# Kernel optimization log

Hardware: AMD Instinct MI355X
Metric: run time of the kernel (lower is better)

The kernel has to match this reference:

```python
import jax, jax.numpy as jnp
import numpy as np

B, T, C, HS = 4, 4096, 1024, 64


def setup_inputs() -> dict:
    key = jax.random.key(0)
    kx, kq, kk, kv = jax.random.split(key, 4)
    x = jax.random.normal(kx, (B, T, C), dtype=jnp.float32)
    s = 1.0 / np.sqrt(C)
    Wq = jax.random.normal(kq, (C, HS), dtype=jnp.float32) * s
    Wk = jax.random.normal(kk, (C, HS), dtype=jnp.float32) * s
    Wv = jax.random.normal(kv, (C, HS), dtype=jnp.float32) * s
    return {"x": x, "Wq": Wq, "Wk": Wk, "Wv": Wv}


def reference(x, Wq, Wk, Wv):
    # q,k,v: [B, T, HS]
    q = x @ Wq
    k = x @ Wk
    v = x @ Wv
    scale = k.shape[-1] ** -0.5
    # full T x T causal attention scores, as the torch module materializes
    scores = jnp.einsum('bqh,bkh->bqk', q, k) * scale  # [B, T, T]
    t = x.shape[1]
    causal = jnp.tril(jnp.ones((t, t), dtype=bool))
    scores = jnp.where(causal[None, :, :], scores, -jnp.inf)
    wei = jax.nn.softmax(scores, axis=-1)  # dropout = 0.0 (eval)
    out = jnp.einsum('bqk,bkh->bqh', wei, v)  # [B, T, HS]
    return out
```

## Files before the change

kernel.cpp:

```cpp
#include <hip/hip_runtime.h>
#include <math.h>

#define BB 4
#define TT 4096
#define CC 1024
#define HS 64
#define MM (BB*TT)
#define KSPLIT 8

typedef __attribute__((ext_vector_type(8))) short short8;
typedef __attribute__((ext_vector_type(4))) float f32x4;
typedef __attribute__((ext_vector_type(4))) unsigned short ushort4v;

__device__ __forceinline__ unsigned short f2bf(float f) {
    union { float f; unsigned u; } v; v.f = f;
    return (unsigned short)((v.u + 0x7fffu + ((v.u >> 16) & 1u)) >> 16);
}

__device__ __forceinline__ unsigned cvt_pk_bf16(float lo, float hi) {
    unsigned r;
    asm("v_cvt_pk_bf16_f32 %0, %1, %2" : "=v"(r) : "v"(lo), "v"(hi));
    return r;
}

__global__ __launch_bounds__(256) void prep_kernel(
    const float* __restrict__ Wq, const float* __restrict__ Wk,
    const float* __restrict__ Wv, unsigned short* __restrict__ Wt)
{
    const int which = blockIdx.x >> 4;
    const int k0 = (blockIdx.x & 15) * 64;
    const float* __restrict__ W = (which == 0) ? Wq : (which == 1) ? Wk : Wv;
    const float scale = (which == 0) ? 0.125f : 1.0f;
    __shared__ unsigned short lds[64][65];
    const int t = threadIdx.x;
    #pragma unroll
    for (int i = 0; i < 16; i++) {
        int idx = t + 256 * i;
        int r = idx >> 6, n = idx & 63;
        lds[r][n] = f2bf(W[(size_t)(k0 + r) * 64 + n] * scale);
    }
    __syncthreads();
    #pragma unroll
    for (int i = 0; i < 16; i++) {
        int idx = t + 256 * i;
        int n = idx >> 6, r = idx & 63;
        Wt[(which << 16) + (n << 10) + k0 + r] = lds[r][n];
    }
}

__global__ __launch_bounds__(256, 2) void qkv_mfma(
    const float* __restrict__ x, const unsigned short* __restrict__ Wt,
    unsigned short* __restrict__ qb, unsigned short* __restrict__ kb,
    unsigned short* __restrict__ vT)
{
    const int rt = blockIdx.x;
    __shared__ unsigned short xs[32][136];
    __shared__ unsigned short ws[192][136];

    const int t = threadIdx.x;
    const int w = t >> 6;
    const int lane = t & 63;
    const int quad = lane >> 4;
    const int c = lane & 15;

    float4 xreg[4];
    short8 wreg[12];
    #pragma unroll
    for (int i = 0; i < 4; i++) {
        int idx = t + 256 * i;
        int r = idx >> 5, c4 = (idx & 31) * 4;
        xreg[i] = *(const float4*)(x + (size_t)(rt * 32 + r) * CC + c4);
    }
    #pragma unroll
    for (int i = 0; i < 12; i++) {
        int idx = t + 256 * i;
        int n = idx >> 4, c8 = (idx & 15) * 8;
        wreg[i] = *(const short8*)(Wt + (size_t)n * CC + c8);
    }

    f32x4 acc[2][3];
    #pragma unroll
    for (int mt = 0; mt < 2; mt++)
        #pragma unroll
        for (int j = 0; j < 3; j++) acc[mt][j] = (f32x4){0.f, 0.f, 0.f, 0.f};

    for (int k0 = 0; k0 < CC; k0 += 128) {
        __syncthreads();
        #pragma unroll
        for (int i = 0; i < 4; i++) {
            int idx = t + 256 * i;
            int r = idx >> 5, c4 = (idx & 31) * 4;
            ushort4v p = { f2bf(xreg[i].x), f2bf(xreg[i].y), f2bf(xreg[i].z), f2bf(xreg[i].w) };
            *(ushort4v*)&xs[r][c4] = p;
        }
        #pragma unroll
        for (int i = 0; i < 12; i++) {
            int idx = t + 256 * i;
            int n = idx >> 4, c8 = (idx & 15) * 8;
            *(short8*)&ws[n][c8] = wreg[i];
        }
        if (k0 + 128 < CC) {
            #pragma unroll
            for (int i = 0; i < 4; i++) {
                int idx = t + 256 * i;
                int r = idx >> 5, c4 = (idx & 31) * 4;
                xreg[i] = *(const float4*)(x + (size_t)(rt * 32 + r) * CC + k0 + 128 + c4);
            }
            #pragma unroll
            for (int i = 0; i < 12; i++) {
                int idx = t + 256 * i;
                int n = idx >> 4, c8 = (idx & 15) * 8;
                wreg[i] = *(const short8*)(Wt + (size_t)n * CC + k0 + 128 + c8);
            }
        }
        __syncthreads();
        #pragma unroll
        for (int ks = 0; ks < 4; ks++) {
            short8 af[2], bf[3];
            #pragma unroll
            for (int mt = 0; mt < 2; mt++)
                af[mt] = *(const short8*)&xs[16 * mt + c][ks * 32 + quad * 8];
            #pragma unroll
            for (int j = 0; j < 3; j++)
                bf[j] = *(const short8*)&ws[16 * (w + 4 * j) + c][ks * 32 + quad * 8];
            #pragma unroll
            for (int mt = 0; mt < 2; mt++)
                #pragma unroll
                for (int j = 0; j < 3; j++)
                    acc[mt][j] = __builtin_amdgcn_mfma_f32_16x16x32_bf16(af[mt], bf[j], acc[mt][j], 0, 0, 0);
        }
    }

    __syncthreads();
    unsigned short (*vtb)[72] = (unsigned short (*)[72])ws;
    #pragma unroll
    for (int mt = 0; mt < 2; mt++) {
        int grow = rt * 32 + 16 * mt + quad * 4;
        #pragma unroll
        for (int reg = 0; reg < 4; reg++) {
            qb[(size_t)(grow + reg) * HS + 16 * w + c] = f2bf(acc[mt][0][reg]);
            kb[(size_t)(grow + reg) * HS + 16 * w + c] = f2bf(acc[mt][1][reg]);
            vtb[16 * w + c][16 * mt + quad * 4 + reg] = f2bf(acc[mt][2][reg]);
        }
    }
    __syncthreads();
    {
        const int b  = rt >> 7;
        const int t0 = (rt & 127) * 32;
        int d = t >> 2, c8 = (t & 3) * 8;
        short8 v0 = *(const short8*)&vtb[d][c8];
        *(short8*)(vT + (size_t)b * HS * TT + (size_t)d * TT + t0 + c8) = v0;
    }
}

__global__ __launch_bounds__(256, 4) void attn_mfma(
    const unsigned short* __restrict__ qb, const unsigned short* __restrict__ kb,
    const unsigned short* __restrict__ vT, float* __restrict__ Opart,
    float* __restrict__ lpart)
{
    const int bid = blockIdx.x;
    const int qt = (TT / 128 - 1) - (bid >> 5);
    const int j  = (bid >> 2) & 7;
    const int b  = bid & 3;

    __shared__ unsigned short ks[64][72];
    __shared__ unsigned short vt[64][72];
    __shared__ unsigned short ps[4][32][72];

    const int t = threadIdx.x;
    const int w = t >> 6;
    const int lane = t & 63;
    const int quad = lane >> 4;
    const int c = lane & 15;
    const int qrow = qt * 128 + 32 * w;

    short8 aq[2][2];
    #pragma unroll
    for (int mt = 0; mt < 2; mt++)
        #pragma unroll
        for (int kstep = 0; kstep < 2; kstep++)
            aq[mt][kstep] = *(const short8*)(qb + (size_t)(b * TT + qrow + 16 * mt + c) * HS + kstep * 32 + quad * 8);

    const int lastkt = 2 * qt + 1;
    const int nkt = (lastkt >= j) ? ((lastkt - j) >> 3) + 1 : 0;
    const unsigned short* Kb = kb + (size_t)b * TT * HS;
    const unsigned short* Vb = vT + (size_t)b * HS * TT;

    const int srow = t >> 3;
    const int sc8  = (t & 7) * 8;

    short8 kreg[2], vreg[2];
    if (nkt > 0) {
        const int kt0 = j * 64;
        #pragma unroll
        for (int i = 0; i < 2; i++) {
            kreg[i] = *(const short8*)(Kb + (size_t)(kt0 + srow + 32 * i) * HS + sc8);
            vreg[i] = *(const short8*)(Vb + (size_t)(srow + 32 * i) * TT + kt0 + sc8);
        }
    }

    float l[2][4] = {{0.f,0.f,0.f,0.f},{0.f,0.f,0.f,0.f}};
    f32x4 oacc[2][4];
    #pragma unroll
    for (int mt = 0; mt < 2; mt++)
        #pragma unroll
        for (int dt = 0; dt < 4; dt++) oacc[mt][dt] = (f32x4){0.f, 0.f, 0.f, 0.f};

#define SCORE_ST(MASKC) do { \
    _Pragma("unroll") \
    for (int st = 0; st < 4; st++) { \
        f32x4 s[2]; \
        s[0] = (f32x4){0.f,0.f,0.f,0.f}; s[1] = (f32x4){0.f,0.f,0.f,0.f}; \
        _Pragma("unroll") \
        for (int kstep = 0; kstep < 2; kstep++) { \
            short8 bf = *(const short8*)&ks[16 * st + c][kstep * 32 + quad * 8]; \
            s[0] = __builtin_amdgcn_mfma_f32_16x16x32_bf16(aq[0][kstep], bf, s[0], 0, 0, 0); \
            s[1] = __builtin_amdgcn_mfma_f32_16x16x32_bf16(aq[1][kstep], bf, s[1], 0, 0, 0); \
        } \
        _Pragma("unroll") \
        for (int mt = 0; mt < 2; mt++) { \
            _Pragma("unroll") \
            for (int reg = 0; reg < 4; reg++) { \
                int kg = kt0 + 16 * st + c; (void)kg; \
                int qg = qrow + 16 * mt + quad * 4 + reg; (void)qg; \
                float p = (MASKC) ? __expf(s[mt][reg]) : 0.f; \
                s[mt][reg] = p; \
                l[mt][reg] += p; \
            } \
            unsigned p01 = cvt_pk_bf16(s[mt][0], s[mt][1]); \
            unsigned p23 = cvt_pk_bf16(s[mt][2], s[mt][3]); \
            ps[w][16 * mt + quad * 4 + 0][16 * st + c] = (unsigned short)p01; \
            ps[w][16 * mt + quad * 4 + 1][16 * st + c] = (unsigned short)(p01 >> 16); \
            ps[w][16 * mt + quad * 4 + 2][16 * st + c] = (unsigned short)p23; \
            ps[w][16 * mt + quad * 4 + 3][16 * st + c] = (unsigned short)(p23 >> 16); \
        } \
    } } while (0)

    for (int i = 0; i < nkt; i++) {
        const int kt = j + KSPLIT * i;
        const int kt0 = kt * 64;
        __syncthreads();
        #pragma unroll
        for (int ii = 0; ii < 2; ii++) {
            *(short8*)&ks[srow + 32 * ii][sc8] = kreg[ii];
            *(short8*)&vt[srow + 32 * ii][sc8] = vreg[ii];
        }
        __syncthreads();

        if (i + 1 < nkt) {
            const int nb = kt0 + KSPLIT * 64;
            #pragma unroll
            for (int ii = 0; ii < 2; ii++) {
                kreg[ii] = *(const short8*)(Kb + (size_t)(nb + srow + 32 * ii) * HS + sc8);
                vreg[ii] = *(const short8*)(Vb + (size_t)(srow + 32 * ii) * TT + nb + sc8);
            }
        }

        if (kt0 > qrow + 31) continue;

        if (kt >= 2 * qt) {
            SCORE_ST(kg <= qg);
        } else {
            SCORE_ST(1);
        }

        #pragma unroll
        for (int kstep = 0; kstep < 2; kstep++) {
            short8 ap[2];
            #pragma unroll
            for (int mt = 0; mt < 2; mt++)
                ap[mt] = *(const short8*)&ps[w][16 * mt + c][kstep * 32 + quad * 8];
            #pragma unroll
            for (int dt = 0; dt < 4; dt++) {
                short8 bv = *(const short8*)&vt[16 * dt + c][kstep * 32 + quad * 8];
                oacc[0][dt] = __builtin_amdgcn_mfma_f32_16x16x32_bf16(ap[0], bv, oacc[0][dt], 0, 0, 0);
                oacc[1][dt] = __builtin_amdgcn_mfma_f32_16x16x32_bf16(ap[1], bv, oacc[1][dt], 0, 0, 0);
            }
        }
    }
#undef SCORE_ST

    #pragma unroll
    for (int mt = 0; mt < 2; mt++)
        #pragma unroll
        for (int reg = 0; reg < 4; reg++)
            #pragma unroll
            for (int msk = 1; msk < 16; msk <<= 1)
                l[mt][reg] += __shfl_xor(l[mt][reg], msk);

    float* __restrict__ Oj = Opart + (size_t)j * MM * HS;
    #pragma unroll
    for (int mt = 0; mt < 2; mt++)
        #pragma unroll
        for (int dt = 0; dt < 4; dt++)
            #pragma unroll
            for (int reg = 0; reg < 4; reg++)
                Oj[(size_t)(b * TT + qrow + 16 * mt + quad * 4 + reg) * HS + 16 * dt + c] = oacc[mt][dt][reg];
    if (c == 0)
        #pragma unroll
        for (int mt = 0; mt < 2; mt++)
            #pragma unroll
            for (int reg = 0; reg < 4; reg++)
                lpart[(size_t)j * MM + b * TT + qrow + 16 * mt + quad * 4 + reg] = l[mt][reg];
}

__global__ __launch_bounds__(256) void combine_kernel(
    const float* __restrict__ Opart, const float* __restrict__ lpart,
    float* __restrict__ out)
{
    const int id = blockIdx.x * 256 + threadIdx.x;
    const int row = id >> 4;
    float l = 0.f;
    #pragma unroll
    for (int j = 0; j < KSPLIT; j++) l += lpart[(size_t)j * MM + row];
    const float4* O = (const float4*)Opart;
    const size_t stride = (size_t)MM * HS / 4;
    float4 r = {0.f, 0.f, 0.f, 0.f};
    #pragma unroll
    for (int j = 0; j < KSPLIT; j++) {
        float4 a = O[id + (size_t)j * stride];
        r.x += a.x; r.y += a.y; r.z += a.z; r.w += a.w;
    }
    float inv = 1.f / l;
    r.x *= inv; r.y *= inv; r.z *= inv; r.w *= inv;
    ((float4*)out)[id] = r;
}

extern "C" void kernel_launch(void* const* d_in, const int* in_sizes, int n_in,
                              void* d_out, int out_size, void* d_ws, size_t ws_size,
                              hipStream_t stream) {
    const float* x  = (const float*)d_in[0];
    const float* Wq = (const float*)d_in[1];
    const float* Wk = (const float*)d_in[2];
    const float* Wv = (const float*)d_in[3];
    float* out = (float*)d_out;

    unsigned short* Wt   = (unsigned short*)d_ws;
    unsigned short* qbuf = Wt + 3 * 64 * 1024;
    unsigned short* kbuf = qbuf + (size_t)MM * HS;
    unsigned short* vTb  = kbuf + (size_t)MM * HS;
    float* Opart = (float*)(vTb + (size_t)MM * HS);
    float* lpart = Opart + (size_t)KSPLIT * MM * HS;

    prep_kernel<<<48, 256, 0, stream>>>(Wq, Wk, Wv, Wt);
    qkv_mfma<<<MM / 32, 256, 0, stream>>>(x, Wt, qbuf, kbuf, vTb);
    attn_mfma<<<BB * (TT / 128) * KSPLIT, 256, 0, stream>>>(qbuf, kbuf, vTb, Opart, lpart);
    combine_kernel<<<1024, 256, 0, stream>>>(Opart, lpart, out);
}
```

Baseline: 137.4 us.

## Load projection weights straight to LDS with pre-swizzled global layout

```diff
diff --git a/kernel.cpp b/kernel.cpp
--- a/kernel.cpp
+++ b/kernel.cpp
@@ -21,6 +21,12 @@
     unsigned r;
     asm("v_cvt_pk_bf16_f32 %0, %1, %2" : "=v"(r) : "v"(lo), "v"(hi));
     return r;
+}
+
+typedef __attribute__((address_space(3))) unsigned short lds_us;
+typedef __attribute__((address_space(1))) const unsigned short glb_us;
+__device__ __forceinline__ void g2lds16(const unsigned short* g, unsigned short* l) {
+    __builtin_amdgcn_global_load_lds((glb_us*)g, (lds_us*)l, 16, 0, 0);
 }
 
 __global__ __launch_bounds__(256) void prep_kernel(
@@ -44,7 +50,10 @@
     for (int i = 0; i < 16; i++) {
         int idx = t + 256 * i;
         int n = idx >> 6, r = idx & 63;
-        Wt[(which << 16) + (n << 10) + k0 + r] = lds[r][n];
+        int nrow = which * 64 + n;
+        int kg = k0 + r;
+        int ck = kg >> 7, kloc = kg & 127;
+        Wt[(size_t)ck * 24576 + (((nrow << 7) + kloc) ^ ((nrow & 7) << 3))] = lds[r][n];
     }
 }
 
@@ -54,8 +63,8 @@
     unsigned short* __restrict__ vT)
 {
     const int rt = blockIdx.x;
-    __shared__ unsigned short xs[32][136];
-    __shared__ unsigned short ws[192][136];
+    __shared__ __align__(16) unsigned short xs[32][136];
+    __shared__ __align__(16) unsigned short wsf[192 * 128];
 
     const int t = threadIdx.x;
     const int w = t >> 6;
@@ -63,20 +72,16 @@
     const int quad = lane >> 4;
     const int c = lane & 15;
 
+    const int c2x32 = ((c >> 2) & 1) << 5;
+    const int quad2 = quad ^ (c & 3);
+
     float4 xreg[4];
-    short8 wreg[12];
     #pragma unroll
     for (int i = 0; i < 4; i++) {
         int idx = t + 256 * i;
         int r = idx >> 5, c4 = (idx & 31) * 4;
         xreg[i] = *(const float4*)(x + (size_t)(rt * 32 + r) * CC + c4);
     }
-    #pragma unroll
-    for (int i = 0; i < 12; i++) {
-        int idx = t + 256 * i;
-        int n = idx >> 4, c8 = (idx & 15) * 8;
-        wreg[i] = *(const short8*)(Wt + (size_t)n * CC + c8);
-    }
 
     f32x4 acc[2][3];
     #pragma unroll
@@ -84,8 +89,14 @@
         #pragma unroll
         for (int j = 0; j < 3; j++) acc[mt][j] = (f32x4){0.f, 0.f, 0.f, 0.f};
 
-    for (int k0 = 0; k0 < CC; k0 += 128) {
+    for (int ck = 0; ck < 8; ++ck) {
         __syncthreads();
+        {
+            const unsigned short* wgp = Wt + (size_t)ck * 24576 + t * 8;
+            #pragma unroll
+            for (int i = 0; i < 12; i++)
+                g2lds16(wgp + i * 2048, wsf + (i * 256 + w * 64) * 8);
+        }
         #pragma unroll
         for (int i = 0; i < 4; i++) {
             int idx = t + 256 * i;
@@ -93,27 +104,17 @@
             ushort4v p = { f2bf(xreg[i].x), f2bf(xreg[i].y), f2bf(xreg[i].z), f2bf(xreg[i].w) };
             *(ushort4v*)&xs[r][c4] = p;
         }
-        #pragma unroll
-        for (int i = 0; i < 12; i++) {
-            int idx = t + 256 * i;
-            int n = idx >> 4, c8 = (idx & 15) * 8;
-            *(short8*)&ws[n][c8] = wreg[i];
-        }
-        if (k0 + 128 < CC) {
+        __syncthreads();
+
+        if (ck + 1 < 8) {
             #pragma unroll
             for (int i = 0; i < 4; i++) {
                 int idx = t + 256 * i;
                 int r = idx >> 5, c4 = (idx & 31) * 4;
-                xreg[i] = *(const float4*)(x + (size_t)(rt * 32 + r) * CC + k0 + 128 + c4);
+                xreg[i] = *(const float4*)(x + (size_t)(rt * 32 + r) * CC + (ck + 1) * 128 + c4);
             }
-            #pragma unroll
-            for (int i = 0; i < 12; i++) {
-                int idx = t + 256 * i;
-                int n = idx >> 4, c8 = (idx & 15) * 8;
-                wreg[i] = *(const short8*)(Wt + (size_t)n * CC + k0 + 128 + c8);
-            }
-        }
-        __syncthreads();
+        }
+
         #pragma unroll
         for (int ks = 0; ks < 4; ks++) {
             short8 af[2], bf[3];
@@ -122,7 +123,8 @@
                 af[mt] = *(const short8*)&xs[16 * mt + c][ks * 32 + quad * 8];
             #pragma unroll
             for (int j = 0; j < 3; j++)
-                bf[j] = *(const short8*)&ws[16 * (w + 4 * j) + c][ks * 32 + quad * 8];
+                bf[j] = *(const short8*)&wsf[(16 * (w + 4 * j) + c) * 128 +
+                                             ((ks * 32) ^ c2x32) + quad2 * 8];
             #pragma unroll
             for (int mt = 0; mt < 2; mt++)
                 #pragma unroll
@@ -132,7 +134,7 @@
     }
 
     __syncthreads();
-    unsigned short (*vtb)[72] = (unsigned short (*)[72])ws;
+    unsigned short (*vtb)[72] = (unsigned short (*)[72])wsf;
     #pragma unroll
     for (int mt = 0; mt < 2; mt++) {
         int grow = rt * 32 + 16 * mt + quad * 4;
```

Result: faster. 134.6 us (-2.0%).
